# Kernel tuning notes

Hardware: AMD Instinct MI355X
Metric: run time of the kernel (lower is better)

## Reference

```python
import jax, jax.numpy as jnp
import numpy as np

B = 256      # batch size (molecules)
A = 64       # num_atoms per molecule
N = B * A    # total nodes = 16384
E = 262144   # num edges
H = 128      # hidden_dim
L = 4        # num_layers
LAT = 64     # latent_dim
AF = 16      # atom_feature_dim
LN_EPS = 1e-5


def setup_inputs() -> dict:
    key = jax.random.key(0)
    ks = jax.random.split(key, 26)
    w = lambda k, shape: (jax.random.normal(k, shape) * 0.05).astype(jnp.float32)
    inp = {}
    inp["z"] = jax.random.normal(ks[0], (B, LAT), jnp.float32)
    inp["atom_types"] = jax.nn.one_hot(
        jax.random.randint(ks[1], (N,), 0, AF), AF, dtype=jnp.float32)
    inp["pos0"] = jax.random.normal(ks[2], (N, 3), jnp.float32) * 0.1
    inp["edge_index"] = jax.random.randint(ks[3], (2, E), 0, N)
    # latent injector: Linear(LAT+AF, 2H) -> SiLU -> Linear(2H, H) -> SiLU -> Linear(H, H)
    inp["inj_W1"] = w(ks[4], (AF + LAT, 2 * H)); inp["inj_b1"] = jnp.zeros((2 * H,), jnp.float32)
    inp["inj_W2"] = w(ks[5], (2 * H, H));        inp["inj_b2"] = jnp.zeros((H,), jnp.float32)
    inp["inj_W3"] = w(ks[6], (H, H));            inp["inj_b3"] = jnp.zeros((H,), jnp.float32)
    # per-layer params, stacked over layer dim L
    inp["edge_W1"] = w(ks[7], (L, 2 * H + 1, H)); inp["edge_b1"] = jnp.zeros((L, H), jnp.float32)
    inp["edge_W2"] = w(ks[8], (L, H, H));         inp["edge_b2"] = jnp.zeros((L, H), jnp.float32)
    inp["coord_W1"] = w(ks[9], (L, H, H));        inp["coord_b1"] = jnp.zeros((L, H), jnp.float32)
    inp["coord_W2"] = w(ks[10], (L, H, 1))  # no bias
    inp["node_W1"] = w(ks[11], (L, 2 * H, H));    inp["node_b1"] = jnp.zeros((L, H), jnp.float32)
    inp["node_W2"] = w(ks[12], (L, H, H));        inp["node_b2"] = jnp.zeros((L, H), jnp.float32)
    inp["ln_g"] = jnp.ones((L, H), jnp.float32)
    inp["ln_b"] = jnp.zeros((L, H), jnp.float32)
    return inp


def _layer_norm(x, g, b):
    mu = jnp.mean(x, axis=-1, keepdims=True)
    var = jnp.mean((x - mu) ** 2, axis=-1, keepdims=True)
    return (x - mu) * jax.lax.rsqrt(var + LN_EPS) * g + b


def _egnn_layer(h, pos, row, col, eW1, eb1, eW2, eb2, cW1, cb1, cW2, nW1, nb1, nW2, nb2, g, b):
    # --- message: gather endpoints, edge MLP ---
    rel = pos[row] - pos[col]                                   # [E, 3]
    dsq = jnp.clip(jnp.sum(rel * rel, axis=1, keepdims=True), 1e-6, 1e6)  # [E, 1]
    ef = jnp.concatenate([h[row], h[col], dsq], axis=1)         # [E, 2H+1]
    m = jax.nn.silu(ef @ eW1 + eb1)
    m = jax.nn.silu(m @ eW2 + eb2)
    m = jnp.clip(m, -10.0, 10.0)                                # [E, H]
    # --- coordinate update: coord MLP -> weighted rel_pos -> scatter_add, mean-normalized ---
    cw = jax.nn.silu(m @ cW1 + cb1) @ cW2                       # [E, 1]
    coord_update = jax.ops.segment_sum(cw * rel, row, num_segments=N)   # [N, 3]
    num_neighbors = jax.ops.segment_sum(jnp.ones((row.shape[0],), m.dtype), row, num_segments=N)[:, None]
    pos_new = pos + coord_update / (num_neighbors + 1e-6)
    # --- node update: scatter_add messages, node MLP, residual + LayerNorm ---
    agg = jax.ops.segment_sum(m, row, num_segments=N)           # [N, H]
    nu = jnp.concatenate([h, agg], axis=1)                      # [N, 2H]
    nu = jax.nn.silu(nu @ nW1 + nb1) @ nW2 + nb2
    h_new = _layer_norm(h + nu, g, b)
    return h_new, pos_new


def reference(z, atom_types, pos0, edge_index,
              inj_W1, inj_b1, inj_W2, inj_b2, inj_W3, inj_b3,
              edge_W1, edge_b1, edge_W2, edge_b2,
              coord_W1, coord_b1, coord_W2,
              node_W1, node_b1, node_W2, node_b2,
              ln_g, ln_b):
    # latent injection: h = MLP(cat[atom_types, repeat_interleave(z, num_atoms)])
    z_exp = jnp.repeat(z, A, axis=0)                            # [N, LAT]
    h = jnp.concatenate([atom_types, z_exp], axis=1)            # [N, AF+LAT]
    h = jax.nn.silu(h @ inj_W1 + inj_b1)
    h = jax.nn.silu(h @ inj_W2 + inj_b2)
    h = h @ inj_W3 + inj_b3                                     # [N, H]
    pos = pos0
    row, col = edge_index[0], edge_index[1]
    for l in range(L):
        h, pos = _egnn_layer(h, pos, row, col,
                             edge_W1[l], edge_b1[l], edge_W2[l], edge_b2[l],
                             coord_W1[l], coord_b1[l], coord_W2[l],
                             node_W1[l], node_b1[l], node_W2[l], node_b2[l],
                             ln_g[l], ln_b[l])
    return pos
```

## Files before the change

kernel.cpp:

```cpp
#include <hip/hip_runtime.h>
#include <cmath>

#define N_NODES 16384
#define E_EDGES 262144
#define HD 128
#define NLAYER 4

typedef __attribute__((ext_vector_type(8))) short bf16x8;
typedef __attribute__((ext_vector_type(4))) float f32x4;
#define MFMA16(a, b, c) __builtin_amdgcn_mfma_f32_16x16x32_bf16(a, b, c, 0, 0, 0)

__device__ __forceinline__ float silu_f(float x) { return x / (1.0f + expf(-x)); }

__device__ __forceinline__ unsigned short bf16_rn(float f) {
  union { float f; unsigned u; } v; v.f = f;
  unsigned r = (v.u + 0x7FFFu + ((v.u >> 16) & 1u)) >> 16;
  return (unsigned short)r;
}
__device__ __forceinline__ float bf16_tof(unsigned short h) {
  union { unsigned u; float f; } v; v.u = ((unsigned)h) << 16; return v.f;
}

__global__ void k_prep_w(const float* __restrict__ eW1, const float* __restrict__ eW2,
                         const float* __restrict__ cW1,
                         unsigned short* __restrict__ e1f, unsigned short* __restrict__ e2f,
                         unsigned short* __restrict__ c1f) {
  int sid = blockIdx.x * 256 + threadIdx.x;
  int layer = sid >> 13;
  int r = sid & 8191;
  const float* src; unsigned short* base; int c, s, halfstride;
  if (r < 4096) {
    c = r >> 9; s = r & 511;
    src = eW1 + (size_t)layer * 257 * 128;
    base = e1f + (size_t)layer * 65536; halfstride = 32768;
  } else if (r < 6144) {
    int rr = r - 4096; c = rr >> 9; s = rr & 511;
    src = eW2 + (size_t)layer * 128 * 128;
    base = e2f + (size_t)layer * 32768; halfstride = 16384;
  } else {
    int rr = r - 6144; c = rr >> 9; s = rr & 511;
    src = cW1 + (size_t)layer * 128 * 128;
    base = c1f + (size_t)layer * 32768; halfstride = 16384;
  }
  int cf = s >> 6, lp = s & 63;
  int n = cf * 16 + (lp & 15);
  int k0 = c * 32 + (lp >> 4) * 8;
  bf16x8 hv, lv;
#pragma unroll
  for (int j = 0; j < 8; ++j) {
    float w = src[(size_t)(k0 + j) * 128 + n];
    unsigned short h = bf16_rn(w);
    hv[j] = (short)h;
    lv[j] = (short)bf16_rn(w - bf16_tof(h));
  }
  size_t off = ((size_t)c * 512 + s) * 8;
  *(bf16x8*)(base + off) = hv;
  *(bf16x8*)(base + halfstride + off) = lv;
}

__global__ void k_h2bf(const float* __restrict__ h, unsigned short* __restrict__ hhi,
                       unsigned short* __restrict__ hlo) {
  int i = (blockIdx.x * 256 + threadIdx.x) * 8;
  float4 a = *(const float4*)(h + i), b = *(const float4*)(h + i + 4);
  float v[8] = {a.x, a.y, a.z, a.w, b.x, b.y, b.z, b.w};
  bf16x8 hv, lv;
#pragma unroll
  for (int j = 0; j < 8; ++j) {
    unsigned short t = bf16_rn(v[j]);
    hv[j] = (short)t;
    lv[j] = (short)bf16_rn(v[j] - bf16_tof(t));
  }
  *(bf16x8*)(hhi + i) = hv;
  *(bf16x8*)(hlo + i) = lv;
}

__global__ __launch_bounds__(256, 3) void k_edge_mfma(
    const unsigned short* __restrict__ hhi, const unsigned short* __restrict__ hlo,
    const float* __restrict__ pos,
    const int* __restrict__ rows, const int* __restrict__ cols, const int* __restrict__ perm,
    const unsigned short* __restrict__ e1f, const float* __restrict__ eW1,
    const float* __restrict__ eb1,
    const unsigned short* __restrict__ e2f, const float* __restrict__ eb2,
    const unsigned short* __restrict__ c1f, const float* __restrict__ cb1,
    const float* __restrict__ cW2,
    float* __restrict__ m_s, float* __restrict__ rel_s, float* __restrict__ cw_s) {
  __shared__ __align__(16) float T[64][132];
  __shared__ __align__(16) short Bl[2][4096];
  __shared__ int srow[64], scol[64];
  __shared__ float sdsq[64];

  const int tid = threadIdx.x;
  const int lane = tid & 63;
  const int w = tid >> 6;
  const int l15 = lane & 15, l4 = lane >> 4;
  const int j0 = blockIdx.x * 64;
  const f32x4 zero4 = {0.f, 0.f, 0.f, 0.f};

  if (tid < 64) {
    int e = perm[j0 + tid];
    int r = rows[e], c = cols[e];
    srow[tid] = r; scol[tid] = c;
    float rx = pos[r * 3 + 0] - pos[c * 3 + 0];
    float ry = pos[r * 3 + 1] - pos[c * 3 + 1];
    float rz = pos[r * 3 + 2] - pos[c * 3 + 2];
    rel_s[(size_t)(j0 + tid) * 3 + 0] = rx;
    rel_s[(size_t)(j0 + tid) * 3 + 1] = ry;
    rel_s[(size_t)(j0 + tid) * 3 + 2] = rz;
    float d = rx * rx + ry * ry + rz * rz;
    sdsq[tid] = fminf(fmaxf(d, 1e-6f), 1e6f);
  }

  f32x4 acc[8];

#pragma unroll
  for (int i = 0; i < 8; ++i) acc[i] = zero4;
  for (int c = 0; c < 8; ++c) {
    __syncthreads();
#pragma unroll
    for (int t = 0; t < 4; ++t) {
      int slot = tid + t * 256;
      int half = slot >> 9, rem = slot & 511;
      const unsigned short* src = e1f + (size_t)half * 32768 + ((size_t)c * 512 + rem) * 8;
      *(bf16x8*)(&Bl[half][rem * 8]) = *(const bf16x8*)src;
    }
    __syncthreads();
    int node = (c < 4 ? srow : scol)[16 * w + l15];
    int koff = (c & 3) * 32 + l4 * 8;
    bf16x8 ah = *(const bf16x8*)(hhi + (size_t)node * 128 + koff);
    bf16x8 al = *(const bf16x8*)(hlo + (size_t)node * 128 + koff);
#pragma unroll
    for (int cf = 0; cf < 8; ++cf) {
      bf16x8 bh = *(const bf16x8*)(&Bl[0][cf * 512 + lane * 8]);
      bf16x8 bl = *(const bf16x8*)(&Bl[1][cf * 512 + lane * 8]);
      acc[cf] = MFMA16(ah, bh, acc[cf]);
      acc[cf] = MFMA16(al, bh, acc[cf]);
      acc[cf] = MFMA16(ah, bl, acc[cf]);
    }
  }
#pragma unroll
  for (int cf = 0; cf < 8; ++cf) {
    int col = cf * 16 + l15;
    float wl = eW1[256 * 128 + col];
    float bb = eb1[col];
#pragma unroll
    for (int r = 0; r < 4; ++r) {
      int trow = 16 * w + l4 * 4 + r;
      T[trow][col] = silu_f(acc[cf][r] + sdsq[trow] * wl + bb);
    }
  }

#pragma unroll
  for (int i = 0; i < 8; ++i) acc[i] = zero4;
  for (int c = 0; c < 4; ++c) {
    __syncthreads();
#pragma unroll
    for (int t = 0; t < 4; ++t) {
      int slot = tid + t * 256;
      int half = slot >> 9, rem = slot & 511;
      const unsigned short* src = e2f + (size_t)half * 16384 + ((size_t)c * 512 + rem) * 8;
      *(bf16x8*)(&Bl[half][rem * 8]) = *(const bf16x8*)src;
    }
    __syncthreads();
    int trow = 16 * w + l15;
    int k0 = c * 32 + l4 * 8;
    float tv[8];
    *(float4*)(tv) = *(const float4*)(&T[trow][k0]);
    *(float4*)(tv + 4) = *(const float4*)(&T[trow][k0 + 4]);
    bf16x8 ah, al;
#pragma unroll
    for (int j = 0; j < 8; ++j) {
      unsigned short t = bf16_rn(tv[j]);
      ah[j] = (short)t;
      al[j] = (short)bf16_rn(tv[j] - bf16_tof(t));
    }
#pragma unroll
    for (int cf = 0; cf < 8; ++cf) {
      bf16x8 bh = *(const bf16x8*)(&Bl[0][cf * 512 + lane * 8]);
      bf16x8 bl = *(const bf16x8*)(&Bl[1][cf * 512 + lane * 8]);
      acc[cf] = MFMA16(ah, bh, acc[cf]);
      acc[cf] = MFMA16(al, bh, acc[cf]);
      acc[cf] = MFMA16(ah, bl, acc[cf]);
    }
  }
#pragma unroll
  for (int cf = 0; cf < 8; ++cf) {
    int col = cf * 16 + l15;
    float bb = eb2[col];
#pragma unroll
    for (int r = 0; r < 4; ++r) {
      int trow = 16 * w + l4 * 4 + r;
      float v = silu_f(acc[cf][r] + bb);
      v = fminf(fmaxf(v, -10.0f), 10.0f);
      m_s[(size_t)(j0 + trow) * 128 + col] = v;
      T[trow][col] = v;
    }
  }

#pragma unroll
  for (int i = 0; i < 8; ++i) acc[i] = zero4;
  for (int c = 0; c < 4; ++c) {
    __syncthreads();
#pragma unroll
    for (int t = 0; t < 4; ++t) {
      int slot = tid + t * 256;
      int half = slot >> 9, rem = slot & 511;
      const unsigned short* src = c1f + (size_t)half * 16384 + ((size_t)c * 512 + rem) * 8;
      *(bf16x8*)(&Bl[half][rem * 8]) = *(const bf16x8*)src;
    }
    __syncthreads();
    int trow = 16 * w + l15;
    int k0 = c * 32 + l4 * 8;
    float tv[8];
    *(float4*)(tv) = *(const float4*)(&T[trow][k0]);
    *(float4*)(tv + 4) = *(const float4*)(&T[trow][k0 + 4]);
    bf16x8 ah, al;
#pragma unroll
    for (int j = 0; j < 8; ++j) {
      unsigned short t = bf16_rn(tv[j]);
      ah[j] = (short)t;
      al[j] = (short)bf16_rn(tv[j] - bf16_tof(t));
    }
#pragma unroll
    for (int cf = 0; cf < 8; ++cf) {
      bf16x8 bh = *(const bf16x8*)(&Bl[0][cf * 512 + lane * 8]);
      bf16x8 bl = *(const bf16x8*)(&Bl[1][cf * 512 + lane * 8]);
      acc[cf] = MFMA16(ah, bh, acc[cf]);
      acc[cf] = MFMA16(al, bh, acc[cf]);
      acc[cf] = MFMA16(ah, bl, acc[cf]);
    }
  }
  {
    float p[4] = {0.f, 0.f, 0.f, 0.f};
#pragma unroll
    for (int cf = 0; cf < 8; ++cf) {
      int col = cf * 16 + l15;
      float bb = cb1[col];
      float w2 = cW2[col];
#pragma unroll
      for (int r = 0; r < 4; ++r) p[r] += silu_f(acc[cf][r] + bb) * w2;
    }
#pragma unroll
    for (int d = 1; d < 16; d <<= 1) {
#pragma unroll
      for (int r = 0; r < 4; ++r) p[r] += __shfl_xor(p[r], d);
    }
    if (l15 == 0) {
#pragma unroll
      for (int r = 0; r < 4; ++r) cw_s[j0 + 16 * w + l4 * 4 + r] = p[r];
    }
  }
}

template <int ACT>
__global__ __launch_bounds__(256, 2) void k_gemm128(const float* Ag, const float* __restrict__ W,
                                                    const float* __restrict__ bias, float* C, int K) {
  __shared__ float As[64][33];
  __shared__ float Ws[32][128];
  const int tid = threadIdx.x;
  const int tc = tid & 15, tr = tid >> 4;
  const int tr4 = tr * 4, tc4 = tc * 4;
  const int m0 = blockIdx.x * 64;

  float acc[4][8];
#pragma unroll
  for (int i = 0; i < 4; ++i)
#pragma unroll
    for (int j = 0; j < 8; ++j) acc[i][j] = 0.0f;

  for (int kk = 0; kk < K; kk += 32) {
    int idx = tid;
#pragma unroll
    for (int it = 0; it < 2; ++it, idx += 256) {
      int r = idx >> 3, c4 = (idx & 7) << 2;
      float4 v = *(const float4*)(Ag + (size_t)(m0 + r) * K + kk + c4);
      As[r][c4] = v.x; As[r][c4 + 1] = v.y; As[r][c4 + 2] = v.z; As[r][c4 + 3] = v.w;
    }
    idx = tid;
#pragma unroll
    for (int it = 0; it < 4; ++it, idx += 256) {
      int r = idx >> 5, c4 = (idx & 31) << 2;
      *(float4*)(&Ws[r][c4]) = *(const float4*)(W + (size_t)(kk + r) * 128 + c4);
    }
    __syncthreads();
#pragma unroll
    for (int k = 0; k < 32; ++k) {
      float av[4];
#pragma unroll
      for (int i = 0; i < 4; ++i) av[i] = As[tr4 + i][k];
      float4 b0 = *(const float4*)(&Ws[k][tc4]);
      float4 b1 = *(const float4*)(&Ws[k][64 + tc4]);
      float bv[8] = {b0.x, b0.y, b0.z, b0.w, b1.x, b1.y, b1.z, b1.w};
#pragma unroll
      for (int i = 0; i < 4; ++i)
#pragma unroll
        for (int j = 0; j < 8; ++j) acc[i][j] = fmaf(av[i], bv[j], acc[i][j]);
    }
    __syncthreads();
  }

  float bv0[8];
#pragma unroll
  for (int j = 0; j < 4; ++j) { bv0[j] = bias[tc4 + j]; bv0[4 + j] = bias[64 + tc4 + j]; }
#pragma unroll
  for (int i = 0; i < 4; ++i) {
    size_t row = m0 + tr4 + i;
    float o[8];
#pragma unroll
    for (int j = 0; j < 8; ++j) {
      float v = acc[i][j] + bv0[j];
      if (ACT >= 1) v = silu_f(v);
      o[j] = v;
    }
    *(float4*)(C + row * 128 + tc4) = make_float4(o[0], o[1], o[2], o[3]);
    *(float4*)(C + row * 128 + 64 + tc4) = make_float4(o[4], o[5], o[6], o[7]);
  }
}

__global__ void k_count(const int* __restrict__ rows, int* __restrict__ cnt) {
  int e = blockIdx.x * 256 + threadIdx.x;
  if (e < E_EDGES) atomicAdd(&cnt[rows[e]], 1);
}

__global__ void k_scan(const int* __restrict__ cnt, int* __restrict__ offs) {
  __shared__ int part[256];
  const int tid = threadIdx.x;
  const int base = tid * 64;
  int s = 0;
  for (int i = 0; i < 64; ++i) s += cnt[base + i];
  part[tid] = s;
  __syncthreads();
  for (int d = 1; d < 256; d <<= 1) {
    int v = (tid >= d) ? part[tid - d] : 0;
    __syncthreads();
    part[tid] += v;
    __syncthreads();
  }
  int run = part[tid] - s;
  for (int i = 0; i < 64; ++i) { offs[base + i] = run; run += cnt[base + i]; }
  if (tid == 255) offs[N_NODES] = run;
}

__global__ void k_fill(const int* __restrict__ rows, const int* __restrict__ offs,
                       int* __restrict__ fill, int* __restrict__ perm) {
  int e = blockIdx.x * 256 + threadIdx.x;
  if (e < E_EDGES) {
    int r = rows[e];
    int p = atomicAdd(&fill[r], 1);
    perm[offs[r] + p] = e;
  }
}

__global__ void k_node_gather(const float* __restrict__ m_s, const float* __restrict__ cw_s,
                              const float* __restrict__ rel_s, const int* __restrict__ offs,
                              float* __restrict__ agg, float* __restrict__ pos) {
  const int node = blockIdx.x * 2 + (threadIdx.x >> 7);
  const int c = threadIdx.x & 127;
  const int o0 = offs[node], o1 = offs[node + 1];
  float s0 = 0.f, s1 = 0.f, s2 = 0.f, s3 = 0.f;
  int j = o0;
  for (; j + 4 <= o1; j += 4) {
    s0 += m_s[(size_t)j * 128 + c];
    s1 += m_s[(size_t)(j + 1) * 128 + c];
    s2 += m_s[(size_t)(j + 2) * 128 + c];
    s3 += m_s[(size_t)(j + 3) * 128 + c];
  }
  for (; j < o1; ++j) s0 += m_s[(size_t)j * 128 + c];
  agg[(size_t)node * 128 + c] = (s0 + s1) + (s2 + s3);
  if (c < 3) {
    float cu = 0.0f;
    for (int jj = o0; jj < o1; ++jj) cu += cw_s[jj] * rel_s[(size_t)jj * 3 + c];
    float deg = (float)(o1 - o0);
    pos[node * 3 + c] += cu / (deg + 1e-6f);
  }
}

__global__ __launch_bounds__(256, 2) void k_node_mlp(float* __restrict__ h, const float* __restrict__ agg,
                                                     const float* __restrict__ W1, const float* __restrict__ b1,
                                                     const float* __restrict__ W2, const float* __restrict__ b2,
                                                     const float* __restrict__ lng, const float* __restrict__ lnb) {
  __shared__ float As[64][33];
  __shared__ float Ws[32][128];
  __shared__ float T[64][132];
  const int tid = threadIdx.x;
  const int tc = tid & 15, tr = tid >> 4;
  const int tr4 = tr * 4, tc4 = tc * 4;
  const int m0 = blockIdx.x * 64;

  float acc[4][8];
#pragma unroll
  for (int i = 0; i < 4; ++i)
#pragma unroll
    for (int j = 0; j < 8; ++j) acc[i][j] = 0.0f;

  for (int kk = 0; kk < 256; kk += 32) {
    const float* src = (kk < 128) ? h : agg;
    const int kb = kk & 127;
    int idx = tid;
#pragma unroll
    for (int it = 0; it < 2; ++it, idx += 256) {
      int r = idx >> 3, c4 = (idx & 7) << 2;
      float4 v = *(const float4*)(src + (size_t)(m0 + r) * 128 + kb + c4);
      As[r][c4] = v.x; As[r][c4 + 1] = v.y; As[r][c4 + 2] = v.z; As[r][c4 + 3] = v.w;
    }
    idx = tid;
#pragma unroll
    for (int it = 0; it < 4; ++it, idx += 256) {
      int r = idx >> 5, c4 = (idx & 31) << 2;
      *(float4*)(&Ws[r][c4]) = *(const float4*)(W1 + (size_t)(kk + r) * 128 + c4);
    }
    __syncthreads();
#pragma unroll
    for (int k = 0; k < 32; ++k) {
      float av[4];
#pragma unroll
      for (int i = 0; i < 4; ++i) av[i] = As[tr4 + i][k];
      float4 b0 = *(const float4*)(&Ws[k][tc4]);
      float4 b1v = *(const float4*)(&Ws[k][64 + tc4]);
      float bv[8] = {b0.x, b0.y, b0.z, b0.w, b1v.x, b1v.y, b1v.z, b1v.w};
#pragma unroll
      for (int i = 0; i < 4; ++i)
#pragma unroll
        for (int j = 0; j < 8; ++j) acc[i][j] = fmaf(av[i], bv[j], acc[i][j]);
    }
    __syncthreads();
  }
#pragma unroll
  for (int i = 0; i < 4; ++i) {
#pragma unroll
    for (int j = 0; j < 4; ++j) {
      T[tr4 + i][tc4 + j] = silu_f(acc[i][j] + b1[tc4 + j]);
      T[tr4 + i][64 + tc4 + j] = silu_f(acc[i][4 + j] + b1[64 + tc4 + j]);
    }
  }
  __syncthreads();

  float acc2[4][8];
#pragma unroll
  for (int i = 0; i < 4; ++i)
#pragma unroll
    for (int j = 0; j < 8; ++j) acc2[i][j] = 0.0f;
  for (int kk = 0; kk < 128; kk += 32) {
    int idx = tid;
#pragma unroll
    for (int it = 0; it < 4; ++it, idx += 256) {
      int r = idx >> 5, c4 = (idx & 31) << 2;
      *(float4*)(&Ws[r][c4]) = *(const float4*)(W2 + (size_t)(kk + r) * 128 + c4);
    }
    __syncthreads();
#pragma unroll
    for (int k = 0; k < 32; ++k) {
      float av[4];
#pragma unroll
      for (int i = 0; i < 4; ++i) av[i] = T[tr4 + i][kk + k];
      float4 b0 = *(const float4*)(&Ws[k][tc4]);
      float4 b1v = *(const float4*)(&Ws[k][64 + tc4]);
      float bv[8] = {b0.x, b0.y, b0.z, b0.w, b1v.x, b1v.y, b1v.z, b1v.w};
#pragma unroll
      for (int i = 0; i < 4; ++i)
#pragma unroll
        for (int j = 0; j < 8; ++j) acc2[i][j] = fmaf(av[i], bv[j], acc2[i][j]);
    }
    __syncthreads();
  }

  float x[4][8], s1[4], s2[4];
#pragma unroll
  for (int i = 0; i < 4; ++i) {
    size_t row = m0 + tr4 + i;
    float4 h0 = *(const float4*)(h + row * 128 + tc4);
    float4 h1 = *(const float4*)(h + row * 128 + 64 + tc4);
    float hv[8] = {h0.x, h0.y, h0.z, h0.w, h1.x, h1.y, h1.z, h1.w};
    s1[i] = 0.f; s2[i] = 0.f;
#pragma unroll
    for (int j = 0; j < 8; ++j) {
      int cidx = (j < 4) ? (tc4 + j) : (64 + tc4 + (j - 4));
      float v = hv[j] + acc2[i][j] + b2[cidx];
      x[i][j] = v;
      s1[i] += v;
      s2[i] += v * v;
    }
  }
#pragma unroll
  for (int d = 1; d < 16; d <<= 1) {
#pragma unroll
    for (int i = 0; i < 4; ++i) {
      s1[i] += __shfl_xor(s1[i], d);
      s2[i] += __shfl_xor(s2[i], d);
    }
  }
  float gv[8], bvv[8];
#pragma unroll
  for (int j = 0; j < 4; ++j) {
    gv[j] = lng[tc4 + j]; gv[4 + j] = lng[64 + tc4 + j];
    bvv[j] = lnb[tc4 + j]; bvv[4 + j] = lnb[64 + tc4 + j];
  }
#pragma unroll
  for (int i = 0; i < 4; ++i) {
    float mu = s1[i] * (1.0f / 128.0f);
    float var = s2[i] * (1.0f / 128.0f) - mu * mu;
    float rs = rsqrtf(var + 1e-5f);
    size_t row = m0 + tr4 + i;
    float o[8];
#pragma unroll
    for (int j = 0; j < 8; ++j) o[j] = (x[i][j] - mu) * rs * gv[j] + bvv[j];
    *(float4*)(h + row * 128 + tc4) = make_float4(o[0], o[1], o[2], o[3]);
    *(float4*)(h + row * 128 + 64 + tc4) = make_float4(o[4], o[5], o[6], o[7]);
  }
}

__global__ __launch_bounds__(256) void k_inj1(const float* __restrict__ at, const float* __restrict__ z,
                                              const float* __restrict__ W1, const float* __restrict__ b1,
                                              float* __restrict__ out) {
  __shared__ float As[64][84];
  __shared__ float Ws[80][128];
  const int tid = threadIdx.x;
  const int tc = tid & 15, tr = tid >> 4;
  const int tr4 = tr * 4, tc4 = tc * 4;
  const int m0 = blockIdx.y * 64;
  const int cb = blockIdx.x * 128;

  int idx = tid;
#pragma unroll
  for (int it = 0; it < 5; ++it, idx += 256) {
    int r = idx / 20, c4 = idx % 20;
    int n = m0 + r;
    float4 v;
    if (c4 < 4) v = *(const float4*)(at + (size_t)n * 16 + c4 * 4);
    else v = *(const float4*)(z + (size_t)(n >> 6) * 64 + (c4 - 4) * 4);
    *(float4*)(&As[r][c4 * 4]) = v;
  }
  idx = tid;
#pragma unroll
  for (int it = 0; it < 10; ++it, idx += 256) {
    int r = idx >> 5, c4 = (idx & 31) << 2;
    *(float4*)(&Ws[r][c4]) = *(const float4*)(W1 + (size_t)r * 256 + cb + c4);
  }
  __syncthreads();

  float acc[4][8];
#pragma unroll
  for (int i = 0; i < 4; ++i)
#pragma unroll
    for (int j = 0; j < 8; ++j) acc[i][j] = 0.0f;
#pragma unroll 4
  for (int k = 0; k < 80; ++k) {
    float av[4];
#pragma unroll
    for (int i = 0; i < 4; ++i) av[i] = As[tr4 + i][k];
    float4 b0 = *(const float4*)(&Ws[k][tc4]);
    float4 b1v = *(const float4*)(&Ws[k][64 + tc4]);
    float bv[8] = {b0.x, b0.y, b0.z, b0.w, b1v.x, b1v.y, b1v.z, b1v.w};
#pragma unroll
    for (int i = 0; i < 4; ++i)
#pragma unroll
      for (int j = 0; j < 8; ++j) acc[i][j] = fmaf(av[i], bv[j], acc[i][j]);
  }

  float bb[8];
#pragma unroll
  for (int j = 0; j < 4; ++j) { bb[j] = b1[cb + tc4 + j]; bb[4 + j] = b1[cb + 64 + tc4 + j]; }
#pragma unroll
  for (int i = 0; i < 4; ++i) {
    size_t row = m0 + tr4 + i;
    float o[8];
#pragma unroll
    for (int j = 0; j < 8; ++j) o[j] = silu_f(acc[i][j] + bb[j]);
    *(float4*)(out + row * 256 + cb + tc4) = make_float4(o[0], o[1], o[2], o[3]);
    *(float4*)(out + row * 256 + cb + 64 + tc4) = make_float4(o[4], o[5], o[6], o[7]);
  }
}

__global__ void k_copyf(const float* __restrict__ in, float* __restrict__ out, int n) {
  int i = blockIdx.x * 256 + threadIdx.x;
  if (i < n) out[i] = in[i];
}

extern "C" void kernel_launch(void* const* d_in, const int* in_sizes, int n_in,
                              void* d_out, int out_size, void* d_ws, size_t ws_size,
                              hipStream_t stream) {
  const float* z = (const float*)d_in[0];
  const float* at = (const float*)d_in[1];
  const float* pos0 = (const float*)d_in[2];
  const int* ei = (const int*)d_in[3];
  const float* injW1 = (const float*)d_in[4];
  const float* injb1 = (const float*)d_in[5];
  const float* injW2 = (const float*)d_in[6];
  const float* injb2 = (const float*)d_in[7];
  const float* injW3 = (const float*)d_in[8];
  const float* injb3 = (const float*)d_in[9];
  const float* eW1 = (const float*)d_in[10];
  const float* eb1 = (const float*)d_in[11];
  const float* eW2 = (const float*)d_in[12];
  const float* eb2 = (const float*)d_in[13];
  const float* cW1 = (const float*)d_in[14];
  const float* cb1 = (const float*)d_in[15];
  const float* cW2 = (const float*)d_in[16];
  const float* nW1 = (const float*)d_in[17];
  const float* nb1 = (const float*)d_in[18];
  const float* nW2 = (const float*)d_in[19];
  const float* nb2 = (const float*)d_in[20];
  const float* lng = (const float*)d_in[21];
  const float* lnb = (const float*)d_in[22];

  float* w = (float*)d_ws;
  float* h = w;    w += (size_t)N_NODES * HD;
  float* pos = w;  w += (size_t)N_NODES * 3;
  float* m_s = w;  w += (size_t)E_EDGES * HD;
  float* rel_s = w; w += (size_t)E_EDGES * 3;
  float* cw_s = w; w += (size_t)E_EDGES;
  float* agg = w;  w += (size_t)N_NODES * HD;
  float* t1 = m_s;
  float* t2 = agg;
  unsigned short* hhi = (unsigned short*)agg;
  unsigned short* hlo = hhi + (size_t)N_NODES * HD;
  int* ib = (int*)w;
  int* cnt = ib;  ib += N_NODES;
  int* offs = ib; ib += N_NODES + 1;
  int* fill = ib; ib += N_NODES;
  int* perm = ib; ib += E_EDGES;
  unsigned short* e1f = (unsigned short*)ib;
  unsigned short* e2f = e1f + (size_t)4 * 65536;
  unsigned short* c1f = e2f + (size_t)4 * 32768;

  const int* rowsp = ei;
  const int* colsp = ei + E_EDGES;

  hipMemsetAsync(cnt, 0, N_NODES * sizeof(int), stream);
  hipMemsetAsync(fill, 0, N_NODES * sizeof(int), stream);
  k_count<<<E_EDGES / 256, 256, 0, stream>>>(rowsp, cnt);
  k_scan<<<1, 256, 0, stream>>>(cnt, offs);
  k_fill<<<E_EDGES / 256, 256, 0, stream>>>(rowsp, offs, fill, perm);
  k_copyf<<<(N_NODES * 3 + 255) / 256, 256, 0, stream>>>(pos0, pos, N_NODES * 3);

  k_prep_w<<<128, 256, 0, stream>>>(eW1, eW2, cW1, e1f, e2f, c1f);

  k_inj1<<<dim3(2, N_NODES / 64), 256, 0, stream>>>(at, z, injW1, injb1, t1);
  k_gemm128<1><<<N_NODES / 64, 256, 0, stream>>>(t1, injW2, injb2, t2, 256);
  k_gemm128<0><<<N_NODES / 64, 256, 0, stream>>>(t2, injW3, injb3, h, 128);

  for (int l = 0; l < NLAYER; ++l) {
    k_h2bf<<<(N_NODES * HD / 8) / 256, 256, 0, stream>>>(h, hhi, hlo);
    k_edge_mfma<<<E_EDGES / 64, 256, 0, stream>>>(
        hhi, hlo, pos, rowsp, colsp, perm,
        e1f + (size_t)l * 65536, eW1 + (size_t)l * 257 * HD, eb1 + l * HD,
        e2f + (size_t)l * 32768, eb2 + l * HD,
        c1f + (size_t)l * 32768, cb1 + l * HD,
        cW2 + (size_t)l * HD,
        m_s, rel_s, cw_s);
    k_node_gather<<<N_NODES / 2, 256, 0, stream>>>(m_s, cw_s, rel_s, offs, agg, pos);
    k_node_mlp<<<N_NODES / 64, 256, 0, stream>>>(h, agg, nW1 + (size_t)l * 2 * HD * HD, nb1 + l * HD,
                                                 nW2 + (size_t)l * HD * HD, nb2 + l * HD,
                                                 lng + l * HD, lnb + l * HD);
  }
  k_copyf<<<(N_NODES * 3 + 255) / 256, 256, 0, stream>>>(pos, (float*)d_out, N_NODES * 3);
}
```

Measured before the change: 1.170 ms.

## Fuse segmented scatter-add of messages and coord updates into edge kernel

The edge kernel now reduces messages and coordinate contributions per destination node inside each 16-row wave tile, using the row-sorted edge order, and atomically adds them into zeroed node buffers. This replaces the per-edge m_s, rel_s and cw_s writes and the separate gather kernel, removing a large per-edge intermediate round trip through memory. A small kernel divides the coordinate sums by degree. It also truncates the hi part of the bf16 split instead of rounding it, and switches SiLU to fast exp and divide intrinsics. In exchange it adds atomics, non-deterministic summation order and two memsets per layer.

```diff
diff --git a/kernel.cpp b/kernel.cpp
--- a/kernel.cpp
+++ b/kernel.cpp
@@ -10,7 +10,9 @@
 typedef __attribute__((ext_vector_type(4))) float f32x4;
 #define MFMA16(a, b, c) __builtin_amdgcn_mfma_f32_16x16x32_bf16(a, b, c, 0, 0, 0)
 
-__device__ __forceinline__ float silu_f(float x) { return x / (1.0f + expf(-x)); }
+__device__ __forceinline__ float silu_f(float x) {
+  return __fdividef(x, 1.0f + __expf(-x));
+}
 
 __device__ __forceinline__ unsigned short bf16_rn(float f) {
   union { float f; unsigned u; } v; v.f = f;
@@ -66,9 +68,10 @@
   bf16x8 hv, lv;
 #pragma unroll
   for (int j = 0; j < 8; ++j) {
-    unsigned short t = bf16_rn(v[j]);
-    hv[j] = (short)t;
-    lv[j] = (short)bf16_rn(v[j] - bf16_tof(t));
+    unsigned u = __float_as_uint(v[j]);
+    hv[j] = (short)(u >> 16);
+    float hi_f = __uint_as_float(u & 0xFFFF0000u);
+    lv[j] = (short)bf16_rn(v[j] - hi_f);
   }
   *(bf16x8*)(hhi + i) = hv;
   *(bf16x8*)(hlo + i) = lv;
@@ -83,11 +86,12 @@
     const unsigned short* __restrict__ e2f, const float* __restrict__ eb2,
     const unsigned short* __restrict__ c1f, const float* __restrict__ cb1,
     const float* __restrict__ cW2,
-    float* __restrict__ m_s, float* __restrict__ rel_s, float* __restrict__ cw_s) {
+    float* __restrict__ agg, float* __restrict__ coordacc) {
   __shared__ __align__(16) float T[64][132];
   __shared__ __align__(16) short Bl[2][4096];
   __shared__ int srow[64], scol[64];
   __shared__ float sdsq[64];
+  __shared__ float srel[64][4];
 
   const int tid = threadIdx.x;
   const int lane = tid & 63;
@@ -103,9 +107,7 @@
     float rx = pos[r * 3 + 0] - pos[c * 3 + 0];
     float ry = pos[r * 3 + 1] - pos[c * 3 + 1];
     float rz = pos[r * 3 + 2] - pos[c * 3 + 2];
-    rel_s[(size_t)(j0 + tid) * 3 + 0] = rx;
-    rel_s[(size_t)(j0 + tid) * 3 + 1] = ry;
-    rel_s[(size_t)(j0 + tid) * 3 + 2] = rz;
+    srel[tid][0] = rx; srel[tid][1] = ry; srel[tid][2] = rz;
     float d = rx * rx + ry * ry + rz * rz;
     sdsq[tid] = fminf(fmaxf(d, 1e-6f), 1e6f);
   }
@@ -169,9 +171,10 @@
     bf16x8 ah, al;
 #pragma unroll
     for (int j = 0; j < 8; ++j) {
-      unsigned short t = bf16_rn(tv[j]);
-      ah[j] = (short)t;
-      al[j] = (short)bf16_rn(tv[j] - bf16_tof(t));
+      unsigned u = __float_as_uint(tv[j]);
+      ah[j] = (short)(u >> 16);
+      float hi_f = __uint_as_float(u & 0xFFFF0000u);
+      al[j] = (short)bf16_rn(tv[j] - hi_f);
     }
 #pragma unroll
     for (int cf = 0; cf < 8; ++cf) {
@@ -191,8 +194,29 @@
       int trow = 16 * w + l4 * 4 + r;
       float v = silu_f(acc[cf][r] + bb);
       v = fminf(fmaxf(v, -10.0f), 10.0f);
-      m_s[(size_t)(j0 + trow) * 128 + col] = v;
+      acc[cf][r] = v;
       T[trow][col] = v;
+    }
+  }
+  {
+    int seg = 0;
+    while (seg < 16) {
+      int node = srow[16 * w + seg];
+      int se = seg + 1;
+      while (se < 16 && srow[16 * w + se] == node) ++se;
+#pragma unroll
+      for (int cf = 0; cf < 8; ++cf) {
+        float s = 0.f;
+#pragma unroll
+        for (int r = 0; r < 4; ++r) {
+          int row = l4 * 4 + r;
+          s += (row >= seg && row < se) ? acc[cf][r] : 0.f;
+        }
+        s += __shfl_xor(s, 16);
+        s += __shfl_xor(s, 32);
+        if (l4 == 0) atomicAdd(&agg[(size_t)node * 128 + cf * 16 + l15], s);
+      }
+      seg = se;
     }
   }
 
@@ -216,9 +240,10 @@
     bf16x8 ah, al;
 #pragma unroll
     for (int j = 0; j < 8; ++j) {
-      unsigned short t = bf16_rn(tv[j]);
-      ah[j] = (short)t;
-      al[j] = (short)bf16_rn(tv[j] - bf16_tof(t));
+      unsigned u = __float_as_uint(tv[j]);
+      ah[j] = (short)(u >> 16);
+      float hi_f = __uint_as_float(u & 0xFFFF0000u);
+      al[j] = (short)bf16_rn(tv[j] - hi_f);
     }
 #pragma unroll
     for (int cf = 0; cf < 8; ++cf) {
@@ -244,10 +269,36 @@
 #pragma unroll
       for (int r = 0; r < 4; ++r) p[r] += __shfl_xor(p[r], d);
     }
-    if (l15 == 0) {
-#pragma unroll
-      for (int r = 0; r < 4; ++r) cw_s[j0 + 16 * w + l4 * 4 + r] = p[r];
-    }
+    int seg = 0;
+    while (seg < 16) {
+      int node = srow[16 * w + seg];
+      int se = seg + 1;
+      while (se < 16 && srow[16 * w + se] == node) ++se;
+      float s = 0.f;
+      if (l15 < 3) {
+#pragma unroll
+        for (int r = 0; r < 4; ++r) {
+          int row = l4 * 4 + r;
+          s += (row >= seg && row < se) ? p[r] * srel[16 * w + row][l15] : 0.f;
+        }
+      }
+      s += __shfl_xor(s, 16);
+      s += __shfl_xor(s, 32);
+      if (l4 == 0 && l15 < 3) atomicAdd(&coordacc[(size_t)node * 4 + l15], s);
+      seg = se;
+    }
+  }
+}
+
+__global__ void k_pos_fin(const float* __restrict__ coordacc, const int* __restrict__ offs,
+                          float* __restrict__ pos) {
+  int n = blockIdx.x * 256 + threadIdx.x;
+  if (n < N_NODES) {
+    float deg = (float)(offs[n + 1] - offs[n]);
+    float inv = __fdividef(1.0f, deg + 1e-6f);
+    pos[n * 3 + 0] += coordacc[n * 4 + 0] * inv;
+    pos[n * 3 + 1] += coordacc[n * 4 + 1] * inv;
+    pos[n * 3 + 2] += coordacc[n * 4 + 2] * inv;
   }
 }
 
@@ -347,30 +398,6 @@
     int r = rows[e];
     int p = atomicAdd(&fill[r], 1);
     perm[offs[r] + p] = e;
-  }
-}
-
-__global__ void k_node_gather(const float* __restrict__ m_s, const float* __restrict__ cw_s,
-                              const float* __restrict__ rel_s, const int* __restrict__ offs,
-                              float* __restrict__ agg, float* __restrict__ pos) {
-  const int node = blockIdx.x * 2 + (threadIdx.x >> 7);
-  const int c = threadIdx.x & 127;
-  const int o0 = offs[node], o1 = offs[node + 1];
-  float s0 = 0.f, s1 = 0.f, s2 = 0.f, s3 = 0.f;
-  int j = o0;
-  for (; j + 4 <= o1; j += 4) {
-    s0 += m_s[(size_t)j * 128 + c];
-    s1 += m_s[(size_t)(j + 1) * 128 + c];
-    s2 += m_s[(size_t)(j + 2) * 128 + c];
-    s3 += m_s[(size_t)(j + 3) * 128 + c];
-  }
-  for (; j < o1; ++j) s0 += m_s[(size_t)j * 128 + c];
-  agg[(size_t)node * 128 + c] = (s0 + s1) + (s2 + s3);
-  if (c < 3) {
-    float cu = 0.0f;
-    for (int jj = o0; jj < o1; ++jj) cu += cw_s[jj] * rel_s[(size_t)jj * 3 + c];
-    float deg = (float)(o1 - o0);
-    pos[node * 3 + c] += cu / (deg + 1e-6f);
   }
 }
 
@@ -603,24 +630,22 @@
   const float* lnb = (const float*)d_in[22];
 
   float* w = (float*)d_ws;
-  float* h = w;    w += (size_t)N_NODES * HD;
-  float* pos = w;  w += (size_t)N_NODES * 3;
-  float* m_s = w;  w += (size_t)E_EDGES * HD;
-  float* rel_s = w; w += (size_t)E_EDGES * 3;
-  float* cw_s = w; w += (size_t)E_EDGES;
-  float* agg = w;  w += (size_t)N_NODES * HD;
-  float* t1 = m_s;
-  float* t2 = agg;
-  unsigned short* hhi = (unsigned short*)agg;
+  float* h = w;        w += (size_t)N_NODES * HD;
+  float* pos = w;      w += (size_t)N_NODES * 3;
+  float* agg = w;      w += (size_t)N_NODES * HD;
+  float* coordacc = w; w += (size_t)N_NODES * 4;
+  float* t1 = w;       w += (size_t)N_NODES * 256;
+  float* t2 = w;       w += (size_t)N_NODES * HD;
+  unsigned short* hhi = (unsigned short*)w;
   unsigned short* hlo = hhi + (size_t)N_NODES * HD;
-  int* ib = (int*)w;
+  unsigned short* e1f = hlo + (size_t)N_NODES * HD;
+  unsigned short* e2f = e1f + (size_t)4 * 65536;
+  unsigned short* c1f = e2f + (size_t)4 * 32768;
+  int* ib = (int*)(c1f + (size_t)4 * 32768);
   int* cnt = ib;  ib += N_NODES;
   int* offs = ib; ib += N_NODES + 1;
   int* fill = ib; ib += N_NODES;
   int* perm = ib; ib += E_EDGES;
-  unsigned short* e1f = (unsigned short*)ib;
-  unsigned short* e2f = e1f + (size_t)4 * 65536;
-  unsigned short* c1f = e2f + (size_t)4 * 32768;
 
   const int* rowsp = ei;
   const int* colsp = ei + E_EDGES;
@@ -639,6 +664,8 @@
   k_gemm128<0><<<N_NODES / 64, 256, 0, stream>>>(t2, injW3, injb3, h, 128);
 
   for (int l = 0; l < NLAYER; ++l) {
+    hipMemsetAsync(agg, 0, (size_t)N_NODES * HD * sizeof(float), stream);
+    hipMemsetAsync(coordacc, 0, (size_t)N_NODES * 4 * sizeof(float), stream);
     k_h2bf<<<(N_NODES * HD / 8) / 256, 256, 0, stream>>>(h, hhi, hlo);
     k_edge_mfma<<<E_EDGES / 64, 256, 0, stream>>>(
         hhi, hlo, pos, rowsp, colsp, perm,
@@ -646,8 +673,8 @@
         e2f + (size_t)l * 32768, eb2 + l * HD,
         c1f + (size_t)l * 32768, cb1 + l * HD,
         cW2 + (size_t)l * HD,
-        m_s, rel_s, cw_s);
-    k_node_gather<<<N_NODES / 2, 256, 0, stream>>>(m_s, cw_s, rel_s, offs, agg, pos);
+        agg, coordacc);
+    k_pos_fin<<<N_NODES / 256, 256, 0, stream>>>(coordacc, offs, pos);
     k_node_mlp<<<N_NODES / 64, 256, 0, stream>>>(h, agg, nW1 + (size_t)l * 2 * HD * HD, nb1 + l * HD,
                                                  nW2 + (size_t)l * HD * HD, nb2 + l * HD,
                                                  lng + l * HD, lnb + l * HD);
```

New measurement: 1.088 ms. 1.08x faster.
